# Performance work log

Measured on AMD Instinct MI355X. Metric: run time of the kernel, lower is better.

Reference implementation:

```python
import jax, jax.numpy as jnp
import numpy as np

NEG = 16          # negative_samples
SKIP = 1          # skip_step


def setup_inputs() -> dict:
    key = jax.random.key(0)
    k1, k2, k3, k4 = jax.random.split(key, 4)
    B, C, H, Wd = 16, 256, 32, 32
    K = 5
    maxN = (H - SKIP - 1) * Wd * B          # largest y'*x*B (k=1)
    z = jax.random.normal(k1, (B, C, H, Wd), dtype=jnp.float32)
    c = jax.random.normal(k2, (B, C, H, Wd), dtype=jnp.float32)
    # 1x1 conv weights W_k: [K, out, in]; scaled so scores are O(1)
    W = jax.random.normal(k3, (K, C, C), dtype=jnp.float32) * (1.0 / C)
    rand_index = jax.random.randint(k4, (K, maxN * NEG), 0, maxN, dtype=jnp.int32)
    return {"z": z, "c": c, "W": W, "rand_index": rand_index}


def reference(z, c, W, rand_index):
    # CLAPP/CPC hinge contrastive loss, contrast_mode='hinge', gating=None,
    # which_update='both', no_gamma=False.
    K = W.shape[0]
    total_loss = jnp.float32(0.0)
    for k in range(1, K + 1):
        # ztwk = W_k(z[:, :, k+skip:, :]) permuted to [y, x, B, C]
        zt = z[:, :, k + SKIP:, :]                              # [B, C, y, x]
        ztwk = jnp.einsum('bcyx,oc->yxbo', zt, W[k - 1])        # [y, x, B, O]
        y, x, b, o = ztwk.shape
        N = y * x * b
        # negative sampling: gather NEG random rows of flattened ztwk
        flat = ztwk.reshape(N, o)
        idx = rand_index[k - 1, :N * NEG] % N                   # in-range indices
        ztwk_shuf = flat[idx].reshape(y, x, b, NEG, o)          # [y, x, B, neg, C]
        # context = c[:, :, :-(k+skip), :] permuted to [y, x, B, C]
        ctx = jnp.transpose(c[:, :, :-(k + SKIP), :], (2, 3, 0, 1))
        scores_pos = jnp.einsum('yxbc,yxbc->yxb', ctx, ztwk)            # [y, x, B]
        scores_neg = jnp.einsum('yxbc,yxbnc->yxbn', ctx, ztwk_shuf)     # [y, x, B, neg]
        # CLAPPHingeLoss (no_gamma=False): clamped hinge terms
        losses_pos = jnp.where(scores_pos < 1.0, 1.0 - scores_pos, 0.0)
        losses_neg = jnp.where(scores_neg > -1.0, 1.0 + scores_neg, 0.0)
        # per-sample means over (neg, y, x) then mean over batch; pos is
        # replicated over neg in the original, which leaves the mean unchanged
        loss_k = losses_pos.mean(axis=(0, 1)).mean() + losses_neg.mean(axis=(0, 1, 3)).mean()
        total_loss = total_loss + loss_k
    return total_loss
```

## Files before the change

### kernel.cpp

```cpp
#include <hip/hip_runtime.h>


typedef unsigned short u16;
typedef unsigned char u8;
typedef unsigned int u32;
typedef __attribute__((ext_vector_type(8))) short bf16x8;
typedef __attribute__((ext_vector_type(4))) float f32x4;
typedef __attribute__((ext_vector_type(2))) float f32x2;

#define NEG_  16
#define MAXN_ 15360
#define TOTROWS 71680
#define NSCORE 17920
#define NPOSP  1120
#define NPARTS (NSCORE + NPOSP)

__device__ __forceinline__ u16 f2bf(float f) {
    union { u32 i; float f; } v; v.f = f;
    u32 b = v.i;
    return (u16)((b + 0x7FFFu + ((b >> 16) & 1u)) >> 16);
}

__device__ __forceinline__ size_t frag_addr(int row, int k) {
    return ((size_t)(row >> 4) * 8 + (k >> 5)) * 512
         + (size_t)((row & 15) + 16 * ((k >> 3) & 3)) * 8 + (k & 7);
}

__global__ __launch_bounds__(256) void transpose_kernel(
    const float* __restrict__ z, const float* __restrict__ cc,
    const float* __restrict__ W,
    u16* __restrict__ ztr, u8* __restrict__ ct8, u16* __restrict__ Wbf)
{
    int tid = threadIdx.x;
    if (blockIdx.z == 2) {
        if (blockIdx.y != 0 || blockIdx.x >= 320) return;
        int i4 = blockIdx.x * 256 + tid;
        float4 v = reinterpret_cast<const float4*>(W)[i4];
        int e = i4 * 4;
        int kw = e >> 16;
        int rem = e & 65535;
        int o = rem >> 8, c = rem & 255;
        size_t base = (size_t)kw * 65536 + frag_addr(o, c);
        ushort4 u;
        u.x = f2bf(v.x); u.y = f2bf(v.y); u.z = f2bf(v.z); u.w = f2bf(v.w);
        *reinterpret_cast<ushort4*>(Wbf + base) = u;
        return;
    }
    int by = blockIdx.x;
    int b = by >> 5, y = by & 31;
    int c0 = blockIdx.y * 64;
    bool is_c = (blockIdx.z == 1);
    if (is_c && y >= 30) return;
    const float* src = is_c ? cc : z;

    __shared__ float ts[64][33];
    int x = tid & 31, ci0 = tid >> 5;
#pragma unroll
    for (int i = 0; i < 8; ++i) {
        int ci = ci0 + i * 8;
        ts[ci][x] = src[(((size_t)b * 256 + c0 + ci) * 32 + y) * 32 + x];
    }
    __syncthreads();
    int cw = tid & 63, xw0 = tid >> 6;
    if (is_c) {
#pragma unroll
        for (int i = 0; i < 8; ++i) {
            int xw = xw0 + i * 4;
            float v = ts[cw][xw];
            u32 pk = __builtin_amdgcn_cvt_pk_fp8_f32(v, v, 0, false);
            ct8[(((size_t)y * 32 + xw) * 16 + b) * 256 + c0 + cw] = (u8)pk;
        }
    } else {
        int k = c0 + cw;
#pragma unroll
        for (int i = 0; i < 8; ++i) {
            int xw = xw0 + i * 4;
            int row = (y * 32 + xw) * 16 + b;
            ztr[frag_addr(row, k)] = f2bf(ts[cw][xw]);
        }
    }
}

__global__ __launch_bounds__(256) void gemm_mfma_kernel(
    const u16* __restrict__ ztr, const u16* __restrict__ Wbf,
    const u8* __restrict__ ct8,
    u8* __restrict__ ztwk8, float* __restrict__ posPart)
{
    int flat = blockIdx.x;
    int kidx, base;
    if (flat < 240)      { kidx = 0; base = 0; }
    else if (flat < 472) { kidx = 1; base = 240; }
    else if (flat < 696) { kidx = 2; base = 472; }
    else if (flat < 912) { kidx = 3; base = 696; }
    else                 { kidx = 4; base = 912; }
    int row0 = (flat - base) * 64;
    int offk = 512 * (30 * kidx - (kidx * (kidx - 1)) / 2);

    int tile0 = (((kidx + 2) * 512 + row0) >> 4);
    const u16* Bsw = Wbf + (size_t)kidx * 65536;
    u8* out = ztwk8 + ((size_t)offk + row0) * 256;

    int wid = threadIdx.x >> 6, lane = threadIdx.x & 63;
    int col0 = wid * 64;

    const u16* Abase = ztr + (size_t)tile0 * 8 * 512 + lane * 8;
    const u16* Bbase = Bsw + (size_t)wid * 4 * 8 * 512 + lane * 8;

    f32x4 acc[4][4] = {};
    bf16x8 a[4], b[4];

#pragma unroll
    for (int i = 0; i < 4; ++i)
        a[i] = *reinterpret_cast<const bf16x8*>(Abase + (size_t)i * 8 * 512);
#pragma unroll
    for (int j = 0; j < 4; ++j)
        b[j] = *reinterpret_cast<const bf16x8*>(Bbase + (size_t)j * 8 * 512);

#pragma unroll
    for (int kb = 0; kb < 8; ++kb) {
        bf16x8 a2[4], b2[4];
        if (kb < 7) {
#pragma unroll
            for (int i = 0; i < 4; ++i)
                a2[i] = *reinterpret_cast<const bf16x8*>(Abase + ((size_t)i * 8 + kb + 1) * 512);
#pragma unroll
            for (int j = 0; j < 4; ++j)
                b2[j] = *reinterpret_cast<const bf16x8*>(Bbase + ((size_t)j * 8 + kb + 1) * 512);
        }
#pragma unroll
        for (int i = 0; i < 4; ++i)
#pragma unroll
            for (int j = 0; j < 4; ++j)
                acc[i][j] = __builtin_amdgcn_mfma_f32_16x16x32_bf16(b[j], a[i], acc[i][j], 0, 0, 0);
        if (kb < 7) {
#pragma unroll
            for (int i = 0; i < 4; ++i) a[i] = a2[i];
#pragma unroll
            for (int j = 0; j < 4; ++j) b[j] = b2[j];
        }
    }

    int lr = lane & 15;
    int rq = (lane >> 4) * 4;
    __shared__ float pos[4][64];

#pragma unroll
    for (int i = 0; i < 4; ++i) {
        int local = row0 + i * 16 + lr;
        float pp = 0.f;
#pragma unroll
        for (int j = 0; j < 4; ++j) {
            u32 u = 0;
            u = __builtin_amdgcn_cvt_pk_fp8_f32(acc[i][j][0], acc[i][j][1], u, false);
            u = __builtin_amdgcn_cvt_pk_fp8_f32(acc[i][j][2], acc[i][j][3], u, true);
            *reinterpret_cast<u32*>(out + (size_t)(i * 16 + lr) * 256 + col0 + j * 16 + rq) = u;
            u32 cw_ = *reinterpret_cast<const u32*>(ct8 + (size_t)local * 256 + col0 + j * 16 + rq);
            f32x2 clo = __builtin_amdgcn_cvt_pk_f32_fp8(cw_, false);
            f32x2 chi = __builtin_amdgcn_cvt_pk_f32_fp8(cw_, true);
            pp = fmaf(acc[i][j][0], clo.x, pp);
            pp = fmaf(acc[i][j][1], clo.y, pp);
            pp = fmaf(acc[i][j][2], chi.x, pp);
            pp = fmaf(acc[i][j][3], chi.y, pp);
        }
        pp += __shfl_xor(pp, 16);
        pp += __shfl_xor(pp, 32);
        if (lane < 16) pos[wid][i * 16 + lane] = pp;
    }
    __syncthreads();

    if (threadIdx.x < 64) {
        float p = pos[0][threadIdx.x] + pos[1][threadIdx.x]
                + pos[2][threadIdx.x] + pos[3][threadIdx.x];
        float Nk = (float)((30 - kidx) * 512);
        float h = fmaxf(0.f, 1.f - p) / Nk;
#pragma unroll
        for (int s = 1; s < 64; s <<= 1) h += __shfl_xor(h, s);
        if (threadIdx.x == 0) posPart[flat] = h;
    }
}

__device__ __forceinline__ float dot16(uint4 nb, const f32x2* cp) {
    f32x2 d0 = {0.f, 0.f}, d1 = {0.f, 0.f};
    d0 += __builtin_amdgcn_cvt_pk_f32_fp8(nb.x, false) * cp[0];
    d1 += __builtin_amdgcn_cvt_pk_f32_fp8(nb.x, true)  * cp[1];
    d0 += __builtin_amdgcn_cvt_pk_f32_fp8(nb.y, false) * cp[2];
    d1 += __builtin_amdgcn_cvt_pk_f32_fp8(nb.y, true)  * cp[3];
    d0 += __builtin_amdgcn_cvt_pk_f32_fp8(nb.z, false) * cp[4];
    d1 += __builtin_amdgcn_cvt_pk_f32_fp8(nb.z, true)  * cp[5];
    d0 += __builtin_amdgcn_cvt_pk_f32_fp8(nb.w, false) * cp[6];
    d1 += __builtin_amdgcn_cvt_pk_f32_fp8(nb.w, true)  * cp[7];
    f32x2 d = d0 + d1;
    return d.x + d.y;
}

__global__ __launch_bounds__(256) void score_kernel(
    const u8* __restrict__ ztwk8, const u8* __restrict__ ct8,
    const int* __restrict__ rind, float* __restrict__ partials)
{
    __shared__ float red[4];
    int bid = blockIdx.x;
    int swb = (bid & 7) * 2240 + (bid >> 3);
    int wid = threadIdx.x >> 6, lane = threadIdx.x & 63;
    int gp = swb * 4 + wid;

    const int ends0 = 15360, ends1 = 30208, ends2 = 44544, ends3 = 58368;
    int kidx, off;
    if (gp < ends0)      { kidx = 0; off = 0; }
    else if (gp < ends1) { kidx = 1; off = ends0; }
    else if (gp < ends2) { kidx = 2; off = ends1; }
    else if (gp < ends3) { kidx = 3; off = ends2; }
    else                 { kidx = 4; off = ends3; }
    int Nk = (30 - kidx) * 512;
    int local = gp - off;

    int r = lane >> 4, c16 = lane & 15;

    const int* rbase = rind + (size_t)kidx * (MAXN_ * NEG_) + (size_t)local * NEG_ + r;
    int rv0 = rbase[0], rv1 = rbase[4], rv2 = rbase[8], rv3 = rbase[12];
    int i0 = rv0 >= Nk ? rv0 - Nk : rv0;
    int i1 = rv1 >= Nk ? rv1 - Nk : rv1;
    int i2 = rv2 >= Nk ? rv2 - Nk : rv2;
    int i3 = rv3 >= Nk ? rv3 - Nk : rv3;

    const u8* zb = ztwk8 + (size_t)off * 256 + c16 * 16;
    uint4 nb0 = *reinterpret_cast<const uint4*>(zb + (size_t)i0 * 256);
    uint4 nb1 = *reinterpret_cast<const uint4*>(zb + (size_t)i1 * 256);
    uint4 nb2 = *reinterpret_cast<const uint4*>(zb + (size_t)i2 * 256);
    uint4 nb3 = *reinterpret_cast<const uint4*>(zb + (size_t)i3 * 256);

    uint4 cw4 = *reinterpret_cast<const uint4*>(ct8 + (size_t)local * 256 + c16 * 16);
    f32x2 cp[8];
    cp[0] = __builtin_amdgcn_cvt_pk_f32_fp8(cw4.x, false);
    cp[1] = __builtin_amdgcn_cvt_pk_f32_fp8(cw4.x, true);
    cp[2] = __builtin_amdgcn_cvt_pk_f32_fp8(cw4.y, false);
    cp[3] = __builtin_amdgcn_cvt_pk_f32_fp8(cw4.y, true);
    cp[4] = __builtin_amdgcn_cvt_pk_f32_fp8(cw4.z, false);
    cp[5] = __builtin_amdgcn_cvt_pk_f32_fp8(cw4.z, true);
    cp[6] = __builtin_amdgcn_cvt_pk_f32_fp8(cw4.w, false);
    cp[7] = __builtin_amdgcn_cvt_pk_f32_fp8(cw4.w, true);

    float d0 = dot16(nb0, cp);
    float d1 = dot16(nb1, cp);
    float d2 = dot16(nb2, cp);
    float d3 = dot16(nb3, cp);

    d0 += __shfl_xor(d0, 1); d1 += __shfl_xor(d1, 1);
    d2 += __shfl_xor(d2, 1); d3 += __shfl_xor(d3, 1);
    d0 += __shfl_xor(d0, 2); d1 += __shfl_xor(d1, 2);
    d2 += __shfl_xor(d2, 2); d3 += __shfl_xor(d3, 2);
    d0 += __shfl_xor(d0, 4); d1 += __shfl_xor(d1, 4);
    d2 += __shfl_xor(d2, 4); d3 += __shfl_xor(d3, 4);
    d0 += __shfl_xor(d0, 8); d1 += __shfl_xor(d1, 8);
    d2 += __shfl_xor(d2, 8); d3 += __shfl_xor(d3, 8);

    float h = fmaxf(0.f, 1.f + d0) + fmaxf(0.f, 1.f + d1)
            + fmaxf(0.f, 1.f + d2) + fmaxf(0.f, 1.f + d3);

    float val = h * (1.0f / 16.0f);
    val += __shfl_xor(val, 16);
    val += __shfl_xor(val, 32);
    val *= 1.0f / (float)Nk;

    if (lane == 0) red[wid] = val;
    __syncthreads();
    if (threadIdx.x == 0)
        partials[bid] = red[0] + red[1] + red[2] + red[3];
}

__global__ __launch_bounds__(1024) void reduce_kernel(
    const float* __restrict__ comb, float* __restrict__ out)
{
    __shared__ float s[16];
    float a = 0.f;
    for (int i = threadIdx.x; i < NPARTS; i += 1024) a += comb[i];
#pragma unroll
    for (int t = 1; t < 64; t <<= 1) a += __shfl_xor(a, t);
    int w = threadIdx.x >> 6, lane = threadIdx.x & 63;
    if (lane == 0) s[w] = a;
    __syncthreads();
    if (threadIdx.x < 16) {
        float v = s[threadIdx.x];
#pragma unroll
        for (int t = 1; t < 16; t <<= 1) v += __shfl_xor(v, t);
        if (threadIdx.x == 0) out[0] = v;
    }
}

extern "C" void kernel_launch(void* const* d_in, const int* in_sizes, int n_in,
                              void* d_out, int out_size, void* d_ws, size_t ws_size,
                              hipStream_t stream) {
    const float* z    = (const float*)d_in[0];
    const float* c    = (const float*)d_in[1];
    const float* W    = (const float*)d_in[2];
    const int*   rind = (const int*)d_in[3];

    char* ws = (char*)d_ws;
    u16*   ztr     = (u16*)  (ws + 0);
    u8*    ct8     = (u8*)   (ws + 8388608);
    u8*    ztwk8   = (u8*)   (ws + 12320768);
    float* parts   = (float*)(ws + 30670848);
    float* posPart = (float*)(ws + 30742528);
    u16*   Wbf     = (u16*)  (ws + 30747008);
    float* out     = (float*)d_out;

    transpose_kernel<<<dim3(512, 4, 3), 256, 0, stream>>>(z, c, W, ztr, ct8, Wbf);
    gemm_mfma_kernel<<<dim3(NPOSP), 256, 0, stream>>>(ztr, Wbf, ct8, ztwk8, posPart);
    score_kernel<<<dim3(NSCORE), 256, 0, stream>>>(ztwk8, ct8, rind, parts);
    reduce_kernel<<<dim3(1), 1024, 0, stream>>>(parts, out);
}
```

Measured before the change: 72.29 us.

## Vectorize bf16 transpose stores, prefetch context in GEMM, drop score block reduction

The transpose kernel now packs eight bf16 values into one 16-byte store per thread in fragment layout, replacing eight scattered 2-byte stores. The GEMM kernel loads its fp8 context values before the MFMA loop so that latency overlaps the matrix work. The score kernel moves to 512-thread blocks and has each wave write its own partial, removing the LDS reduction and barrier. The cost is a larger partial array for the final single-block reduce and more registers held live in the GEMM.

```diff
diff --git a/kernel.cpp b/kernel.cpp
--- a/kernel.cpp
+++ b/kernel.cpp
@@ -11,14 +11,16 @@
 #define NEG_  16
 #define MAXN_ 15360
 #define TOTROWS 71680
-#define NSCORE 17920
 #define NPOSP  1120
-#define NPARTS (NSCORE + NPOSP)
+#define NPARTS (TOTROWS + NPOSP)
 
 __device__ __forceinline__ u16 f2bf(float f) {
     union { u32 i; float f; } v; v.f = f;
     u32 b = v.i;
     return (u16)((b + 0x7FFFu + ((b >> 16) & 1u)) >> 16);
+}
+__device__ __forceinline__ u32 f2bf2(float lo, float hi) {
+    return (u32)f2bf(lo) | ((u32)f2bf(hi) << 16);
 }
 
 __device__ __forceinline__ size_t frag_addr(int row, int k) {
@@ -61,8 +63,8 @@
         ts[ci][x] = src[(((size_t)b * 256 + c0 + ci) * 32 + y) * 32 + x];
     }
     __syncthreads();
-    int cw = tid & 63, xw0 = tid >> 6;
     if (is_c) {
+        int cw = tid & 63, xw0 = tid >> 6;
 #pragma unroll
         for (int i = 0; i < 8; ++i) {
             int xw = xw0 + i * 4;
@@ -71,13 +73,15 @@
             ct8[(((size_t)y * 32 + xw) * 16 + b) * 256 + c0 + cw] = (u8)pk;
         }
     } else {
-        int k = c0 + cw;
-#pragma unroll
-        for (int i = 0; i < 8; ++i) {
-            int xw = xw0 + i * 4;
-            int row = (y * 32 + xw) * 16 + b;
-            ztr[frag_addr(row, k)] = f2bf(ts[cw][xw]);
-        }
+        int g = tid >> 5;
+        int row = (y * 32 + x) * 16 + b;
+        int k0 = c0 + g * 8;
+        uint4 w;
+        w.x = f2bf2(ts[g * 8 + 0][x], ts[g * 8 + 1][x]);
+        w.y = f2bf2(ts[g * 8 + 2][x], ts[g * 8 + 3][x]);
+        w.z = f2bf2(ts[g * 8 + 4][x], ts[g * 8 + 5][x]);
+        w.w = f2bf2(ts[g * 8 + 6][x], ts[g * 8 + 7][x]);
+        *reinterpret_cast<uint4*>(ztr + frag_addr(row, k0)) = w;
     }
 }
 
@@ -102,9 +106,19 @@
 
     int wid = threadIdx.x >> 6, lane = threadIdx.x & 63;
     int col0 = wid * 64;
+    int lr = lane & 15;
+    int rq = (lane >> 4) * 4;
 
     const u16* Abase = ztr + (size_t)tile0 * 8 * 512 + lane * 8;
     const u16* Bbase = Bsw + (size_t)wid * 4 * 8 * 512 + lane * 8;
+
+    u32 cw[4][4];
+#pragma unroll
+    for (int i = 0; i < 4; ++i)
+#pragma unroll
+        for (int j = 0; j < 4; ++j)
+            cw[i][j] = *reinterpret_cast<const u32*>(
+                ct8 + (size_t)(row0 + i * 16 + lr) * 256 + col0 + j * 16 + rq);
 
     f32x4 acc[4][4] = {};
     bf16x8 a[4], b[4];
@@ -140,13 +154,10 @@
         }
     }
 
-    int lr = lane & 15;
-    int rq = (lane >> 4) * 4;
     __shared__ float pos[4][64];
 
 #pragma unroll
     for (int i = 0; i < 4; ++i) {
-        int local = row0 + i * 16 + lr;
         float pp = 0.f;
 #pragma unroll
         for (int j = 0; j < 4; ++j) {
@@ -154,9 +165,8 @@
             u = __builtin_amdgcn_cvt_pk_fp8_f32(acc[i][j][0], acc[i][j][1], u, false);
             u = __builtin_amdgcn_cvt_pk_fp8_f32(acc[i][j][2], acc[i][j][3], u, true);
             *reinterpret_cast<u32*>(out + (size_t)(i * 16 + lr) * 256 + col0 + j * 16 + rq) = u;
-            u32 cw_ = *reinterpret_cast<const u32*>(ct8 + (size_t)local * 256 + col0 + j * 16 + rq);
-            f32x2 clo = __builtin_amdgcn_cvt_pk_f32_fp8(cw_, false);
-            f32x2 chi = __builtin_amdgcn_cvt_pk_f32_fp8(cw_, true);
+            f32x2 clo = __builtin_amdgcn_cvt_pk_f32_fp8(cw[i][j], false);
+            f32x2 chi = __builtin_amdgcn_cvt_pk_f32_fp8(cw[i][j], true);
             pp = fmaf(acc[i][j][0], clo.x, pp);
             pp = fmaf(acc[i][j][1], clo.y, pp);
             pp = fmaf(acc[i][j][2], chi.x, pp);
@@ -193,15 +203,14 @@
     return d.x + d.y;
 }
 
-__global__ __launch_bounds__(256) void score_kernel(
+__global__ __launch_bounds__(512) void score_kernel(
     const u8* __restrict__ ztwk8, const u8* __restrict__ ct8,
     const int* __restrict__ rind, float* __restrict__ partials)
 {
-    __shared__ float red[4];
     int bid = blockIdx.x;
-    int swb = (bid & 7) * 2240 + (bid >> 3);
+    int swb = (bid & 7) * 1120 + (bid >> 3);
     int wid = threadIdx.x >> 6, lane = threadIdx.x & 63;
-    int gp = swb * 4 + wid;
+    int gp = swb * 8 + wid;
 
     const int ends0 = 15360, ends1 = 30208, ends2 = 44544, ends3 = 58368;
     int kidx, off;
@@ -261,10 +270,7 @@
     val += __shfl_xor(val, 32);
     val *= 1.0f / (float)Nk;
 
-    if (lane == 0) red[wid] = val;
-    __syncthreads();
-    if (threadIdx.x == 0)
-        partials[bid] = red[0] + red[1] + red[2] + red[3];
+    if (lane == 0) partials[gp] = val;
 }
 
 __global__ __launch_bounds__(1024) void reduce_kernel(
@@ -299,12 +305,12 @@
     u8*    ct8     = (u8*)   (ws + 8388608);
     u8*    ztwk8   = (u8*)   (ws + 12320768);
     float* parts   = (float*)(ws + 30670848);
-    float* posPart = (float*)(ws + 30742528);
-    u16*   Wbf     = (u16*)  (ws + 30747008);
+    float* posPart = (float*)(ws + 30957568);
+    u16*   Wbf     = (u16*)  (ws + 30962048);
     float* out     = (float*)d_out;
 
     transpose_kernel<<<dim3(512, 4, 3), 256, 0, stream>>>(z, c, W, ztr, ct8, Wbf);
     gemm_mfma_kernel<<<dim3(NPOSP), 256, 0, stream>>>(ztr, Wbf, ct8, ztwk8, posPart);
-    score_kernel<<<dim3(NSCORE), 256, 0, stream>>>(ztwk8, ct8, rind, parts);
+    score_kernel<<<dim3(8960), 512, 0, stream>>>(ztwk8, ct8, rind, parts);
     reduce_kernel<<<dim3(1), 1024, 0, stream>>>(parts, out);
 }
```

New measurement: 90.65 us. 1.25x slower.
